# Kernel tuning notes

Measured on AMD Instinct MI355X. Metric: run time of the kernel, lower is better.

Reference implementation:

```python
import jax, jax.numpy as jnp
import numpy as np

H = 128   # hidden_size
DYN = 2   # dynamic_features


def setup_inputs() -> dict:
    B, S, STAT = 256, 64, 2
    key = jax.random.key(0)
    ks = jax.random.split(key, 9)
    sc = 0.05
    return {
        "static": jax.random.normal(ks[0], (B, STAT, S), jnp.float32),
        "static_embeddings": jax.random.normal(ks[1], (B, H, S), jnp.float32),
        "dynamic": jax.random.uniform(ks[2], (B, DYN, S), jnp.float32),
        # dynamic_embedding: Conv1d(2 -> 128, k=1)
        "dyn_w": jax.random.normal(ks[3], (H, DYN), jnp.float32) * sc,
        "dyn_b": jnp.zeros((H,), jnp.float32),
        # decoder_input_dynamic_embedding: Conv1d(128 -> 128, k=1)
        "in_w": jax.random.normal(ks[4], (H, H), jnp.float32) * sc,
        "in_b": jnp.zeros((H,), jnp.float32),
        # GRU (single layer, batch_first), torch gate order r,z,n
        "w_ih": jax.random.normal(ks[5], (3 * H, H), jnp.float32) * sc,
        "w_hh": jax.random.normal(ks[6], (3 * H, H), jnp.float32) * sc,
        "b_ih": jnp.zeros((3 * H,), jnp.float32),
        "b_hh": jnp.zeros((3 * H,), jnp.float32),
        # DoubleAttention: scores = v . tanh(W [static; dynamic; hidden])
        "W_att": jax.random.normal(ks[7], (H, 3 * H), jnp.float32) * sc,
        "v_att": jax.random.normal(ks[8], (H,), jnp.float32) * sc,
    }


def _pointer_forward(static_embeddings, dynamic, dyn_w, dyn_b, in_w, in_b,
                     w_ih, w_hh, b_ih, b_hh, W_att, v_att):
    B, Hd, S = static_embeddings.shape
    NEG = jnp.asarray(-1e9, static_embeddings.dtype)
    base = jax.random.key(42)

    def gru_cell(x, h):  # torch nn.GRU single step
        gi = x @ w_ih.T + b_ih
        gh = h @ w_hh.T + b_hh
        ir, iz, i_n = jnp.split(gi, 3, axis=-1)
        hr, hz, h_n = jnp.split(gh, 3, axis=-1)
        r = jax.nn.sigmoid(ir + hr)
        z = jax.nn.sigmoid(iz + hz)
        n = jnp.tanh(i_n + r * h_n)
        return (1.0 - z) * n + z * h

    first_mask = jnp.zeros((B, S), static_embeddings.dtype).at[:, 0].set(1.0)

    def step(carry, i):
        dec_in, h, visited, dyn = carry
        # decoder_input_dynamic_embedding: 1x1 conv == per-token linear
        x = dec_in @ in_w.T + in_b                      # [B,H]
        h = gru_cell(x, h)                              # decoder_output == new hidden
        # i==0: only depot (index 0) is selectable; afterwards: unvisited nodes
        mask = jnp.where(i == 0, first_mask, 1.0 - visited)
        dyn_emb = jnp.einsum('bds,hd->bhs', dyn, dyn_w) + dyn_b[None, :, None]
        ctx = jnp.concatenate(
            [static_embeddings, dyn_emb,
             jnp.broadcast_to(h[:, :, None], (B, Hd, S))], axis=1)  # [B,3H,S]
        scores = jnp.einsum('h,bhs->bs', v_att,
                            jnp.tanh(jnp.einsum('hk,bks->bhs', W_att, ctx)))
        logits = jnp.where(mask > 0, scores, NEG)       # -inf on masked positions
        ptr = jax.random.categorical(jax.random.fold_in(base, i), logits)  # sample
        logp = jnp.take_along_axis(jax.nn.log_softmax(logits, -1),
                                   ptr[:, None], axis=1)[:, 0]
        sel = (jnp.arange(S)[None, :] == ptr[:, None]).astype(dyn.dtype)  # [B,S]
        visited = jnp.maximum(visited, sel)
        dyn = dyn * (1.0 - sel)[:, None, :]             # update_dynamic_state
        # original feeds the (conv-transformed) decoder input back to itself
        return (x, h, visited, dyn), (ptr, logp)

    init = (static_embeddings[:, :, 0],                  # decoder_input = emb of node 0
            jnp.zeros((B, Hd), static_embeddings.dtype),  # GRU hidden
            jnp.zeros((B, S), static_embeddings.dtype),   # visited
            dynamic)
    _, (tours, logps) = jax.lax.scan(step, init, jnp.arange(S))
    return tours.T, logps.T  # [B,S], [B,S]


def reference(static, static_embeddings, dynamic, dyn_w, dyn_b, in_w, in_b,
              w_ih, w_hh, b_ih, b_hh, W_att, v_att):
    # dropout layers are identity in eval mode; `static` is only used for logging
    return _pointer_forward(static_embeddings, dynamic, dyn_w, dyn_b, in_w, in_b,
                            w_ih, w_hh, b_ih, b_hh, W_att, v_att)
```

## Files before the change

kernel.cpp:

```cpp
#include <hip/hip_runtime.h>
#include <stdint.h>


#define BN 256
#define SN 64
#define HN 128
#define NEGV (-1.0e9f)
#define TINYF 1.17549435e-38f

#define OFF_A   0
#define OFF_GI  8192
#define OFF_WHC 8192
#define OFF_SET 16384
#define OFF_UT  24832
#define OFF_HC  33280
#define OFF_KK  33536
#define OFF_SV  33664
#define OFF_DY  33792
#define OFF_WD  33920
#define OFF_CV  34176
#define SMEM_FLOATS 34304

__device__ __forceinline__ uint32_t rotl32(uint32_t v, int d) {
  return (v << d) | (v >> (32 - d));
}

__device__ __forceinline__ void threefry2x32(uint32_t k0, uint32_t k1,
                                             uint32_t x0, uint32_t x1,
                                             uint32_t& o0, uint32_t& o1) {
  uint32_t ks2 = k0 ^ k1 ^ 0x1BD11BDAu;
  x0 += k0; x1 += k1;
  x0 += x1; x1 = rotl32(x1, 13); x1 ^= x0;
  x0 += x1; x1 = rotl32(x1, 15); x1 ^= x0;
  x0 += x1; x1 = rotl32(x1, 26); x1 ^= x0;
  x0 += x1; x1 = rotl32(x1, 6);  x1 ^= x0;
  x0 += k1; x1 += ks2 + 1u;
  x0 += x1; x1 = rotl32(x1, 17); x1 ^= x0;
  x0 += x1; x1 = rotl32(x1, 29); x1 ^= x0;
  x0 += x1; x1 = rotl32(x1, 16); x1 ^= x0;
  x0 += x1; x1 = rotl32(x1, 24); x1 ^= x0;
  x0 += ks2; x1 += k0 + 2u;
  x0 += x1; x1 = rotl32(x1, 13); x1 ^= x0;
  x0 += x1; x1 = rotl32(x1, 15); x1 ^= x0;
  x0 += x1; x1 = rotl32(x1, 26); x1 ^= x0;
  x0 += x1; x1 = rotl32(x1, 6);  x1 ^= x0;
  x0 += k0; x1 += k1 + 3u;
  x0 += x1; x1 = rotl32(x1, 17); x1 ^= x0;
  x0 += x1; x1 = rotl32(x1, 29); x1 ^= x0;
  x0 += x1; x1 = rotl32(x1, 16); x1 ^= x0;
  x0 += x1; x1 = rotl32(x1, 24); x1 ^= x0;
  x0 += k1; x1 += ks2 + 4u;
  x0 += x1; x1 = rotl32(x1, 13); x1 ^= x0;
  x0 += x1; x1 = rotl32(x1, 15); x1 ^= x0;
  x0 += x1; x1 = rotl32(x1, 26); x1 ^= x0;
  x0 += x1; x1 = rotl32(x1, 6);  x1 ^= x0;
  x0 += ks2; x1 += k0 + 5u;
  o0 = x0; o1 = x1;
}

__device__ __forceinline__ float jax_gumbel(uint32_t k0, uint32_t k1, int j) {
  uint32_t o0, o1;
  threefry2x32(k0, k1, 0u, (uint32_t)j, o0, o1);
  uint32_t bits = o0 ^ o1;
  uint32_t ub = (bits >> 9) | 0x3F800000u;
  float u = __uint_as_float(ub) - 1.0f;
  u = fmaxf(u + TINYF, TINYF);
  return -logf(-logf(u));
}

__device__ __forceinline__ float ftanh(float x) {
  float ax = fabsf(x);
  float e = __expf(-2.0f * ax);
  float r = (1.0f - e) * __builtin_amdgcn_rcpf(1.0f + e);
  return copysignf(r, x);
}

__device__ __forceinline__ float fsig(float x) {
  return __builtin_amdgcn_rcpf(1.0f + __expf(-x));
}

__global__ void k0_dyn(const float* __restrict__ W_att, const float* __restrict__ dyn_w,
                       const float* __restrict__ dyn_b, float* __restrict__ Wd,
                       float* __restrict__ cv) {
  int h = threadIdx.x;
  float w0 = 0.f, w1 = 0.f, cc = 0.f;
  for (int k = 0; k < HN; ++k) {
    float w = W_att[h * 384 + 128 + k];
    w0 = fmaf(w, dyn_w[2 * k + 0], w0);
    w1 = fmaf(w, dyn_w[2 * k + 1], w1);
    cc = fmaf(w, dyn_b[k], cc);
  }
  Wd[2 * h] = w0; Wd[2 * h + 1] = w1; cv[h] = cc;
}

__global__ __launch_bounds__(512)
__attribute__((amdgpu_waves_per_eu(2, 2)))
void mega(
    const float* __restrict__ SE, const float* __restrict__ dynamic,
    const float* __restrict__ in_w, const float* __restrict__ in_b,
    const float* __restrict__ w_ih, const float* __restrict__ b_ih,
    const float* __restrict__ w_hh, const float* __restrict__ b_hh,
    const float* __restrict__ W_att, const float* __restrict__ v_att,
    const float* __restrict__ Wd, const float* __restrict__ cv,
    float* __restrict__ out) {
  extern __shared__ float sm[];
  int b = blockIdx.x, t = threadIdx.x;
  float* A   = sm + OFF_A;
  float* GIl = sm + OFF_GI;
  float* WHC = sm + OFF_WHC;
  float* SET = sm + OFF_SET;
  float* UT  = sm + OFF_UT;
  float* HC  = sm + OFF_HC;
  uint32_t* KK = (uint32_t*)(sm + OFF_KK);
  float* SV  = sm + OFF_SV;
  float* DY  = sm + OFF_DY;
  float* WDs = sm + OFF_WD;
  float* CVs = sm + OFF_CV;

  if (t < 64) {
    uint32_t o0, o1;
    threefry2x32(0u, 42u, 0u, (uint32_t)t, o0, o1);
    KK[2 * t] = o0; KK[2 * t + 1] = o1;
  }
  if (t < 128) {
    SV[t]  = v_att[t];
    DY[t]  = dynamic[b * 128 + t];
    CVs[t] = cv[t];
    HC[t]  = SE[b * 8192 + t * 64];
  }
  if (t < 256) WDs[t] = Wd[t];
  __syncthreads();

  {
    int ml = t >> 2, ks = t & 3;
    float4 wv[8];
#pragma unroll
    for (int q = 0; q < 8; ++q)
      wv[q] = *(const float4*)(in_w + ml * HN + q * 16 + ks * 4);
    float bib = in_b[ml];
    for (int ii = 0; ii < SN; ++ii) {
      const float* xc = HC + (ii & 1) * 128;
      float* xn = HC + ((ii + 1) & 1) * 128;
      float a0 = 0.f, a1 = 0.f, a2 = 0.f, a3 = 0.f;
#pragma unroll
      for (int q = 0; q < 8; ++q) {
        float4 x4 = *(const float4*)(xc + q * 16 + ks * 4);
        a0 = fmaf(wv[q].x, x4.x, a0);
        a1 = fmaf(wv[q].y, x4.y, a1);
        a2 = fmaf(wv[q].z, x4.z, a2);
        a3 = fmaf(wv[q].w, x4.w, a3);
      }
      float s = (a0 + a1) + (a2 + a3);
      s += __shfl_xor(s, 1); s += __shfl_xor(s, 2);
      if (ks == 0) {
        float xv = s + bib;
        A[ii * 128 + ml] = xv;
        xn[ml] = xv;
      }
      __syncthreads();
    }
  }

  {
    int ml = t >> 2, ks = t & 3;
    float4 wv[3][8]; float bi[3];
#pragma unroll
    for (int j = 0; j < 3; ++j) {
#pragma unroll
      for (int q = 0; q < 8; ++q)
        wv[j][q] = *(const float4*)(w_ih + (ml + 128 * j) * HN + q * 16 + ks * 4);
      bi[j] = b_ih[ml + 128 * j];
    }
    for (int n = 0; n < SN; ++n) {
      float4 x4[8];
#pragma unroll
      for (int q = 0; q < 8; ++q)
        x4[q] = *(const float4*)(A + n * 128 + q * 16 + ks * 4);
      float sum[3];
#pragma unroll
      for (int j = 0; j < 3; ++j) {
        float a0 = 0.f, a1 = 0.f, a2 = 0.f, a3 = 0.f;
#pragma unroll
        for (int q = 0; q < 8; ++q) {
          a0 = fmaf(wv[j][q].x, x4[q].x, a0);
          a1 = fmaf(wv[j][q].y, x4[q].y, a1);
          a2 = fmaf(wv[j][q].z, x4[q].z, a2);
          a3 = fmaf(wv[j][q].w, x4[q].w, a3);
        }
        float s = (a0 + a1) + (a2 + a3);
        s += __shfl_xor(s, 1); s += __shfl_xor(s, 2);
        sum[j] = s + bi[j];
      }
      if (ks == 0) {
#pragma unroll
        for (int j = 0; j < 3; ++j) GIl[n * 384 + ml + 128 * j] = sum[j];
      }
    }
    __syncthreads();
  }

  if (t < 256) HC[t] = 0.f;
  __syncthreads();
  {
    int ml = t >> 2, ks = t & 3;
    float4 wv[3][8]; float bh[3];
#pragma unroll
    for (int j = 0; j < 3; ++j) {
#pragma unroll
      for (int q = 0; q < 8; ++q)
        wv[j][q] = *(const float4*)(w_hh + (ml + 128 * j) * HN + q * 16 + ks * 4);
      bh[j] = b_hh[ml + 128 * j];
    }
    float hp = 0.f;
    for (int ii = 0; ii < SN; ++ii) {
      const float* hcr = HC + (ii & 1) * 128;
      float* hcw = HC + ((ii + 1) & 1) * 128;
      float4 x4[8];
#pragma unroll
      for (int q = 0; q < 8; ++q)
        x4[q] = *(const float4*)(hcr + q * 16 + ks * 4);
      float sum[3];
#pragma unroll
      for (int j = 0; j < 3; ++j) {
        float a0 = 0.f, a1 = 0.f, a2 = 0.f, a3 = 0.f;
#pragma unroll
        for (int q = 0; q < 8; ++q) {
          a0 = fmaf(wv[j][q].x, x4[q].x, a0);
          a1 = fmaf(wv[j][q].y, x4[q].y, a1);
          a2 = fmaf(wv[j][q].z, x4[q].z, a2);
          a3 = fmaf(wv[j][q].w, x4[q].w, a3);
        }
        float s = (a0 + a1) + (a2 + a3);
        s += __shfl_xor(s, 1); s += __shfl_xor(s, 2);
        sum[j] = s + bh[j];
      }
      if (ks == 0) {
        const float* gr = GIl + ii * 384;
        float r = fsig(gr[ml] + sum[0]);
        float z = fsig(gr[128 + ml] + sum[1]);
        float nn = ftanh(gr[256 + ml] + r * sum[2]);
        float hn = (1.0f - z) * nn + z * hp;
        hcw[ml] = hn;
        A[ii * 128 + ml] = hn;
        hp = hn;
      }
      __syncthreads();
    }
  }

  {
    int ml = t >> 3, ks = t & 7;
    float4 w0[4], w1[4];
#pragma unroll
    for (int q = 0; q < 4; ++q) {
      w0[q] = *(const float4*)(W_att + (ml)      * 384 + 256 + q * 32 + ks * 4);
      w1[q] = *(const float4*)(W_att + (ml + 64) * 384 + 256 + q * 32 + ks * 4);
    }
    for (int n = 0; n < SN; ++n) {
      float4 x4[4];
#pragma unroll
      for (int q = 0; q < 4; ++q)
        x4[q] = *(const float4*)(A + n * 128 + q * 32 + ks * 4);
      float a00 = 0.f, a01 = 0.f, a10 = 0.f, a11 = 0.f;
#pragma unroll
      for (int q = 0; q < 4; ++q) {
        a00 = fmaf(w0[q].x, x4[q].x, a00);
        a01 = fmaf(w0[q].y, x4[q].y, a01);
        a00 = fmaf(w0[q].z, x4[q].z, a00);
        a01 = fmaf(w0[q].w, x4[q].w, a01);
        a10 = fmaf(w1[q].x, x4[q].x, a10);
        a11 = fmaf(w1[q].y, x4[q].y, a11);
        a10 = fmaf(w1[q].z, x4[q].z, a10);
        a11 = fmaf(w1[q].w, x4[q].w, a11);
      }
      float s0 = a00 + a01, s1 = a10 + a11;
      s0 += __shfl_xor(s0, 1); s0 += __shfl_xor(s0, 2); s0 += __shfl_xor(s0, 4);
      s1 += __shfl_xor(s1, 1); s1 += __shfl_xor(s1, 2); s1 += __shfl_xor(s1, 4);
      if (ks == 0) { WHC[n * 128 + ml] = s0; WHC[n * 128 + ml + 64] = s1; }
    }
    __syncthreads();
  }

  for (int p = 0; p < 16; ++p) {
    int idx = p * 512 + t;
    int h = idx >> 6, s = idx & 63;
    SET[s * 132 + h] = SE[b * 8192 + idx];
  }
  __syncthreads();

  {
    int ml = t >> 3, ks = t & 7;
    float4 w0[4], w1[4];
#pragma unroll
    for (int q = 0; q < 4; ++q) {
      w0[q] = *(const float4*)(W_att + (ml)      * 384 + q * 32 + ks * 4);
      w1[q] = *(const float4*)(W_att + (ml + 64) * 384 + q * 32 + ks * 4);
    }
    for (int n = 0; n < SN; ++n) {
      float4 x4[4];
#pragma unroll
      for (int q = 0; q < 4; ++q)
        x4[q] = *(const float4*)(SET + n * 132 + q * 32 + ks * 4);
      float a00 = 0.f, a01 = 0.f, a10 = 0.f, a11 = 0.f;
#pragma unroll
      for (int q = 0; q < 4; ++q) {
        a00 = fmaf(w0[q].x, x4[q].x, a00);
        a01 = fmaf(w0[q].y, x4[q].y, a01);
        a00 = fmaf(w0[q].z, x4[q].z, a00);
        a01 = fmaf(w0[q].w, x4[q].w, a01);
        a10 = fmaf(w1[q].x, x4[q].x, a10);
        a11 = fmaf(w1[q].y, x4[q].y, a11);
        a10 = fmaf(w1[q].z, x4[q].z, a10);
        a11 = fmaf(w1[q].w, x4[q].w, a11);
      }
      float s0 = a00 + a01, s1 = a10 + a11;
      s0 += __shfl_xor(s0, 1); s0 += __shfl_xor(s0, 2); s0 += __shfl_xor(s0, 4);
      s1 += __shfl_xor(s1, 1); s1 += __shfl_xor(s1, 2); s1 += __shfl_xor(s1, 4);
      if (ks == 0) {
        float d0 = DY[n], d1 = DY[64 + n];
        UT[(ml)      * 66 + n] = s0 + WDs[2 * ml] * d0 + WDs[2 * ml + 1] * d1 + CVs[ml];
        UT[(ml + 64) * 66 + n] = s1 + WDs[2 * (ml + 64)] * d0 + WDs[2 * (ml + 64) + 1] * d1 + CVs[ml + 64];
      }
    }
    __syncthreads();
  }

  {
    int s = t & 63, w = t >> 6;
    float acc[8];
#pragma unroll
    for (int j = 0; j < 8; ++j) acc[j] = 0.f;
    for (int h = 0; h < HN; h += 4) {
      float u0 = UT[(h + 0) * 66 + s];
      float u1 = UT[(h + 1) * 66 + s];
      float u2 = UT[(h + 2) * 66 + s];
      float u3 = UT[(h + 3) * 66 + s];
      float4 v4 = *(const float4*)(SV + h);
#pragma unroll
      for (int j = 0; j < 8; ++j) {
        float4 wh = *(const float4*)(WHC + (w * 8 + j) * 128 + h);
        float a = acc[j];
        a = fmaf(v4.x, ftanh(u0 + wh.x), a);
        a = fmaf(v4.y, ftanh(u1 + wh.y), a);
        a = fmaf(v4.z, ftanh(u2 + wh.z), a);
        a = fmaf(v4.w, ftanh(u3 + wh.w), a);
        acc[j] = a;
      }
    }
    __syncthreads();
#pragma unroll
    for (int j = 0; j < 8; ++j) A[(w * 8 + j) * 64 + s] = acc[j];
    __syncthreads();
  }

  {
    float* G = A + 4096;
    for (int p = 0; p < 8; ++p) {
      int idx = p * 512 + t;
      int i = idx >> 6;
      G[idx] = jax_gumbel(KK[2 * i], KK[2 * i + 1], b * 64 + (idx & 63));
    }
    __syncthreads();
  }

  if (t < 64) {
    const float* Pl = A;
    const float* Gl = A + 4096;
    int s = t;
    bool visited = false;
    for (int i = 0; i < SN; ++i) {
      float score = Pl[i * 64 + s];
      bool allowed = (i == 0) ? (s == 0) : (!visited);
      float logit = allowed ? score : NEGV;
      float z = logit + Gl[i * 64 + s];
      float bz = z; int bi = s;
#pragma unroll
      for (int off = 32; off > 0; off >>= 1) {
        float oz = __shfl_xor(bz, off);
        int oi = __shfl_xor(bi, off);
        if (oz > bz || (oz == bz && oi < bi)) { bz = oz; bi = oi; }
      }
      int ptr = bi;
      float m = logit;
#pragma unroll
      for (int off = 32; off > 0; off >>= 1) m = fmaxf(m, __shfl_xor(m, off));
      float e = expf(logit - m);
      float sum = e;
#pragma unroll
      for (int off = 32; off > 0; off >>= 1) sum += __shfl_xor(sum, off);
      float chosen = __shfl(logit, ptr);
      float logp = (chosen - m) - logf(sum);
      if (s == ptr) visited = true;
      if (s == 0) {
        out[b * SN + i] = (float)ptr;
        out[BN * SN + b * SN + i] = logp;
      }
    }
  }
}

extern "C" void kernel_launch(void* const* d_in, const int* in_sizes, int n_in,
                              void* d_out, int out_size, void* d_ws, size_t ws_size,
                              hipStream_t stream) {
  const float* SE    = (const float*)d_in[1];
  const float* dynam = (const float*)d_in[2];
  const float* dyn_w = (const float*)d_in[3];
  const float* dyn_b = (const float*)d_in[4];
  const float* in_w  = (const float*)d_in[5];
  const float* in_b  = (const float*)d_in[6];
  const float* w_ih  = (const float*)d_in[7];
  const float* b_ih  = (const float*)d_in[8 - 1];
  const float* w_hh  = (const float*)d_in[8];
  const float* b_ih2 = (const float*)d_in[9];
  const float* b_hh  = (const float*)d_in[10];
  const float* W_att = (const float*)d_in[11];
  const float* v_att = (const float*)d_in[12];
  float* out = (float*)d_out;
  float* ws = (float*)d_ws;

  float* Wd = ws;
  float* cv = ws + 256;

  (void)hipFuncSetAttribute((const void*)mega,
                            hipFuncAttributeMaxDynamicSharedMemorySize,
                            SMEM_FLOATS * 4);

  hipLaunchKernelGGL(k0_dyn, dim3(1), dim3(128), 0, stream,
                     W_att, dyn_w, dyn_b, Wd, cv);
  hipLaunchKernelGGL(mega, dim3(BN), dim3(512), SMEM_FLOATS * 4, stream,
                     SE, dynam, in_w, in_b, w_ih, b_ih2, w_hh, b_hh,
                     W_att, v_att, Wd, cv, out);
}
```

Measured before the change: 317.9 us.

## Double block size to 1024 threads and split each dot product across 8 lanes

Launches the per-batch mega kernel with 1024 threads instead of 512 and re-partitions every matvec phase. Each output row now gets 8 lanes, each holding 4 float4 weight registers, with a three-stage shuffle reduction. The attention projections compute one row per thread group instead of two, and the score loop handles 4 query rows per wave instead of 8. The aim is to halve per-thread work and register load in the serial GRU and input-conv recurrences, which are latency bound. The cost is barriers across 16 waves instead of 8 and an extra shuffle stage per reduction.

```diff
diff --git a/kernel.cpp b/kernel.cpp
--- a/kernel.cpp
+++ b/kernel.cpp
@@ -93,9 +93,7 @@
   Wd[2 * h] = w0; Wd[2 * h + 1] = w1; cv[h] = cc;
 }
 
-__global__ __launch_bounds__(512)
-__attribute__((amdgpu_waves_per_eu(2, 2)))
-void mega(
+__global__ __launch_bounds__(1024) void mega(
     const float* __restrict__ SE, const float* __restrict__ dynamic,
     const float* __restrict__ in_w, const float* __restrict__ in_b,
     const float* __restrict__ w_ih, const float* __restrict__ b_ih,
@@ -117,6 +115,8 @@
   float* WDs = sm + OFF_WD;
   float* CVs = sm + OFF_CV;
 
+  int ml = t >> 3, ks = t & 7;
+
   if (t < 64) {
     uint32_t o0, o1;
     threefry2x32(0u, 42u, 0u, (uint32_t)t, o0, o1);
@@ -132,26 +132,25 @@
   __syncthreads();
 
   {
-    int ml = t >> 2, ks = t & 3;
-    float4 wv[8];
-#pragma unroll
-    for (int q = 0; q < 8; ++q)
-      wv[q] = *(const float4*)(in_w + ml * HN + q * 16 + ks * 4);
+    float4 wv[4];
+#pragma unroll
+    for (int q = 0; q < 4; ++q)
+      wv[q] = *(const float4*)(in_w + ml * HN + q * 32 + ks * 4);
     float bib = in_b[ml];
     for (int ii = 0; ii < SN; ++ii) {
       const float* xc = HC + (ii & 1) * 128;
       float* xn = HC + ((ii + 1) & 1) * 128;
       float a0 = 0.f, a1 = 0.f, a2 = 0.f, a3 = 0.f;
 #pragma unroll
-      for (int q = 0; q < 8; ++q) {
-        float4 x4 = *(const float4*)(xc + q * 16 + ks * 4);
+      for (int q = 0; q < 4; ++q) {
+        float4 x4 = *(const float4*)(xc + q * 32 + ks * 4);
         a0 = fmaf(wv[q].x, x4.x, a0);
         a1 = fmaf(wv[q].y, x4.y, a1);
         a2 = fmaf(wv[q].z, x4.z, a2);
         a3 = fmaf(wv[q].w, x4.w, a3);
       }
       float s = (a0 + a1) + (a2 + a3);
-      s += __shfl_xor(s, 1); s += __shfl_xor(s, 2);
+      s += __shfl_xor(s, 1); s += __shfl_xor(s, 2); s += __shfl_xor(s, 4);
       if (ks == 0) {
         float xv = s + bib;
         A[ii * 128 + ml] = xv;
@@ -162,33 +161,32 @@
   }
 
   {
-    int ml = t >> 2, ks = t & 3;
-    float4 wv[3][8]; float bi[3];
+    float4 wv[3][4]; float bi[3];
 #pragma unroll
     for (int j = 0; j < 3; ++j) {
 #pragma unroll
-      for (int q = 0; q < 8; ++q)
-        wv[j][q] = *(const float4*)(w_ih + (ml + 128 * j) * HN + q * 16 + ks * 4);
+      for (int q = 0; q < 4; ++q)
+        wv[j][q] = *(const float4*)(w_ih + (ml + 128 * j) * HN + q * 32 + ks * 4);
       bi[j] = b_ih[ml + 128 * j];
     }
     for (int n = 0; n < SN; ++n) {
-      float4 x4[8];
-#pragma unroll
-      for (int q = 0; q < 8; ++q)
-        x4[q] = *(const float4*)(A + n * 128 + q * 16 + ks * 4);
+      float4 x4[4];
+#pragma unroll
+      for (int q = 0; q < 4; ++q)
+        x4[q] = *(const float4*)(A + n * 128 + q * 32 + ks * 4);
       float sum[3];
 #pragma unroll
       for (int j = 0; j < 3; ++j) {
         float a0 = 0.f, a1 = 0.f, a2 = 0.f, a3 = 0.f;
 #pragma unroll
-        for (int q = 0; q < 8; ++q) {
+        for (int q = 0; q < 4; ++q) {
           a0 = fmaf(wv[j][q].x, x4[q].x, a0);
           a1 = fmaf(wv[j][q].y, x4[q].y, a1);
           a2 = fmaf(wv[j][q].z, x4[q].z, a2);
           a3 = fmaf(wv[j][q].w, x4[q].w, a3);
         }
         float s = (a0 + a1) + (a2 + a3);
-        s += __shfl_xor(s, 1); s += __shfl_xor(s, 2);
+        s += __shfl_xor(s, 1); s += __shfl_xor(s, 2); s += __shfl_xor(s, 4);
         sum[j] = s + bi[j];
       }
       if (ks == 0) {
@@ -202,36 +200,35 @@
   if (t < 256) HC[t] = 0.f;
   __syncthreads();
   {
-    int ml = t >> 2, ks = t & 3;
-    float4 wv[3][8]; float bh[3];
+    float4 wv[3][4]; float bh[3];
 #pragma unroll
     for (int j = 0; j < 3; ++j) {
 #pragma unroll
-      for (int q = 0; q < 8; ++q)
-        wv[j][q] = *(const float4*)(w_hh + (ml + 128 * j) * HN + q * 16 + ks * 4);
+      for (int q = 0; q < 4; ++q)
+        wv[j][q] = *(const float4*)(w_hh + (ml + 128 * j) * HN + q * 32 + ks * 4);
       bh[j] = b_hh[ml + 128 * j];
     }
     float hp = 0.f;
     for (int ii = 0; ii < SN; ++ii) {
       const float* hcr = HC + (ii & 1) * 128;
       float* hcw = HC + ((ii + 1) & 1) * 128;
-      float4 x4[8];
-#pragma unroll
-      for (int q = 0; q < 8; ++q)
-        x4[q] = *(const float4*)(hcr + q * 16 + ks * 4);
+      float4 x4[4];
+#pragma unroll
+      for (int q = 0; q < 4; ++q)
+        x4[q] = *(const float4*)(hcr + q * 32 + ks * 4);
       float sum[3];
 #pragma unroll
       for (int j = 0; j < 3; ++j) {
         float a0 = 0.f, a1 = 0.f, a2 = 0.f, a3 = 0.f;
 #pragma unroll
-        for (int q = 0; q < 8; ++q) {
+        for (int q = 0; q < 4; ++q) {
           a0 = fmaf(wv[j][q].x, x4[q].x, a0);
           a1 = fmaf(wv[j][q].y, x4[q].y, a1);
           a2 = fmaf(wv[j][q].z, x4[q].z, a2);
           a3 = fmaf(wv[j][q].w, x4[q].w, a3);
         }
         float s = (a0 + a1) + (a2 + a3);
-        s += __shfl_xor(s, 1); s += __shfl_xor(s, 2);
+        s += __shfl_xor(s, 1); s += __shfl_xor(s, 2); s += __shfl_xor(s, 4);
         sum[j] = s + bh[j];
       }
       if (ks == 0) {
@@ -249,77 +246,56 @@
   }
 
   {
-    int ml = t >> 3, ks = t & 7;
-    float4 w0[4], w1[4];
-#pragma unroll
-    for (int q = 0; q < 4; ++q) {
-      w0[q] = *(const float4*)(W_att + (ml)      * 384 + 256 + q * 32 + ks * 4);
-      w1[q] = *(const float4*)(W_att + (ml + 64) * 384 + 256 + q * 32 + ks * 4);
-    }
+    float4 wv[4];
+#pragma unroll
+    for (int q = 0; q < 4; ++q)
+      wv[q] = *(const float4*)(W_att + ml * 384 + 256 + q * 32 + ks * 4);
     for (int n = 0; n < SN; ++n) {
-      float4 x4[4];
-#pragma unroll
-      for (int q = 0; q < 4; ++q)
-        x4[q] = *(const float4*)(A + n * 128 + q * 32 + ks * 4);
-      float a00 = 0.f, a01 = 0.f, a10 = 0.f, a11 = 0.f;
+      float a0 = 0.f, a1 = 0.f, a2 = 0.f, a3 = 0.f;
 #pragma unroll
       for (int q = 0; q < 4; ++q) {
-        a00 = fmaf(w0[q].x, x4[q].x, a00);
-        a01 = fmaf(w0[q].y, x4[q].y, a01);
-        a00 = fmaf(w0[q].z, x4[q].z, a00);
-        a01 = fmaf(w0[q].w, x4[q].w, a01);
-        a10 = fmaf(w1[q].x, x4[q].x, a10);
-        a11 = fmaf(w1[q].y, x4[q].y, a11);
-        a10 = fmaf(w1[q].z, x4[q].z, a10);
-        a11 = fmaf(w1[q].w, x4[q].w, a11);
-      }
-      float s0 = a00 + a01, s1 = a10 + a11;
-      s0 += __shfl_xor(s0, 1); s0 += __shfl_xor(s0, 2); s0 += __shfl_xor(s0, 4);
-      s1 += __shfl_xor(s1, 1); s1 += __shfl_xor(s1, 2); s1 += __shfl_xor(s1, 4);
-      if (ks == 0) { WHC[n * 128 + ml] = s0; WHC[n * 128 + ml + 64] = s1; }
-    }
-    __syncthreads();
-  }
-
-  for (int p = 0; p < 16; ++p) {
-    int idx = p * 512 + t;
+        float4 x4 = *(const float4*)(A + n * 128 + q * 32 + ks * 4);
+        a0 = fmaf(wv[q].x, x4.x, a0);
+        a1 = fmaf(wv[q].y, x4.y, a1);
+        a2 = fmaf(wv[q].z, x4.z, a2);
+        a3 = fmaf(wv[q].w, x4.w, a3);
+      }
+      float s = (a0 + a1) + (a2 + a3);
+      s += __shfl_xor(s, 1); s += __shfl_xor(s, 2); s += __shfl_xor(s, 4);
+      if (ks == 0) WHC[n * 128 + ml] = s;
+    }
+    __syncthreads();
+  }
+
+#pragma unroll
+  for (int p = 0; p < 8; ++p) {
+    int idx = p * 1024 + t;
     int h = idx >> 6, s = idx & 63;
     SET[s * 132 + h] = SE[b * 8192 + idx];
   }
   __syncthreads();
 
   {
-    int ml = t >> 3, ks = t & 7;
-    float4 w0[4], w1[4];
-#pragma unroll
-    for (int q = 0; q < 4; ++q) {
-      w0[q] = *(const float4*)(W_att + (ml)      * 384 + q * 32 + ks * 4);
-      w1[q] = *(const float4*)(W_att + (ml + 64) * 384 + q * 32 + ks * 4);
-    }
+    float4 wv[4];
+#pragma unroll
+    for (int q = 0; q < 4; ++q)
+      wv[q] = *(const float4*)(W_att + ml * 384 + q * 32 + ks * 4);
+    float wd0 = WDs[2 * ml], wd1 = WDs[2 * ml + 1], cvm = CVs[ml];
     for (int n = 0; n < SN; ++n) {
-      float4 x4[4];
-#pragma unroll
-      for (int q = 0; q < 4; ++q)
-        x4[q] = *(const float4*)(SET + n * 132 + q * 32 + ks * 4);
-      float a00 = 0.f, a01 = 0.f, a10 = 0.f, a11 = 0.f;
+      float a0 = 0.f, a1 = 0.f, a2 = 0.f, a3 = 0.f;
 #pragma unroll
       for (int q = 0; q < 4; ++q) {
-        a00 = fmaf(w0[q].x, x4[q].x, a00);
-        a01 = fmaf(w0[q].y, x4[q].y, a01);
-        a00 = fmaf(w0[q].z, x4[q].z, a00);
-        a01 = fmaf(w0[q].w, x4[q].w, a01);
-        a10 = fmaf(w1[q].x, x4[q].x, a10);
-        a11 = fmaf(w1[q].y, x4[q].y, a11);
-        a10 = fmaf(w1[q].z, x4[q].z, a10);
-        a11 = fmaf(w1[q].w, x4[q].w, a11);
-      }
-      float s0 = a00 + a01, s1 = a10 + a11;
-      s0 += __shfl_xor(s0, 1); s0 += __shfl_xor(s0, 2); s0 += __shfl_xor(s0, 4);
-      s1 += __shfl_xor(s1, 1); s1 += __shfl_xor(s1, 2); s1 += __shfl_xor(s1, 4);
+        float4 x4 = *(const float4*)(SET + n * 132 + q * 32 + ks * 4);
+        a0 = fmaf(wv[q].x, x4.x, a0);
+        a1 = fmaf(wv[q].y, x4.y, a1);
+        a2 = fmaf(wv[q].z, x4.z, a2);
+        a3 = fmaf(wv[q].w, x4.w, a3);
+      }
+      float s = (a0 + a1) + (a2 + a3);
+      s += __shfl_xor(s, 1); s += __shfl_xor(s, 2); s += __shfl_xor(s, 4);
       if (ks == 0) {
         float d0 = DY[n], d1 = DY[64 + n];
-        UT[(ml)      * 66 + n] = s0 + WDs[2 * ml] * d0 + WDs[2 * ml + 1] * d1 + CVs[ml];
-        UT[(ml + 64) * 66 + n] = s1 + WDs[2 * (ml + 64)] * d0 + WDs[2 * (ml + 64) + 1] * d1 + CVs[ml + 64];
+        UT[ml * 66 + n] = s + wd0 * d0 + wd1 * d1 + cvm;
       }
     }
     __syncthreads();
@@ -327,9 +303,9 @@
 
   {
     int s = t & 63, w = t >> 6;
-    float acc[8];
-#pragma unroll
-    for (int j = 0; j < 8; ++j) acc[j] = 0.f;
+    float acc[4];
+#pragma unroll
+    for (int j = 0; j < 4; ++j) acc[j] = 0.f;
     for (int h = 0; h < HN; h += 4) {
       float u0 = UT[(h + 0) * 66 + s];
       float u1 = UT[(h + 1) * 66 + s];
@@ -337,8 +313,8 @@
       float u3 = UT[(h + 3) * 66 + s];
       float4 v4 = *(const float4*)(SV + h);
 #pragma unroll
-      for (int j = 0; j < 8; ++j) {
-        float4 wh = *(const float4*)(WHC + (w * 8 + j) * 128 + h);
+      for (int j = 0; j < 4; ++j) {
+        float4 wh = *(const float4*)(WHC + (w * 4 + j) * 128 + h);
         float a = acc[j];
         a = fmaf(v4.x, ftanh(u0 + wh.x), a);
         a = fmaf(v4.y, ftanh(u1 + wh.y), a);
@@ -349,14 +325,15 @@
     }
     __syncthreads();
 #pragma unroll
-    for (int j = 0; j < 8; ++j) A[(w * 8 + j) * 64 + s] = acc[j];
+    for (int j = 0; j < 4; ++j) A[(w * 4 + j) * 64 + s] = acc[j];
     __syncthreads();
   }
 
   {
     float* G = A + 4096;
-    for (int p = 0; p < 8; ++p) {
-      int idx = p * 512 + t;
+#pragma unroll
+    for (int p = 0; p < 4; ++p) {
+      int idx = p * 1024 + t;
       int i = idx >> 6;
       G[idx] = jax_gumbel(KK[2 * i], KK[2 * i + 1], b * 64 + (idx & 63));
     }
@@ -409,9 +386,8 @@
   const float* in_w  = (const float*)d_in[5];
   const float* in_b  = (const float*)d_in[6];
   const float* w_ih  = (const float*)d_in[7];
-  const float* b_ih  = (const float*)d_in[8 - 1];
   const float* w_hh  = (const float*)d_in[8];
-  const float* b_ih2 = (const float*)d_in[9];
+  const float* b_ih  = (const float*)d_in[9];
   const float* b_hh  = (const float*)d_in[10];
   const float* W_att = (const float*)d_in[11];
   const float* v_att = (const float*)d_in[12];
@@ -427,7 +403,7 @@
 
   hipLaunchKernelGGL(k0_dyn, dim3(1), dim3(128), 0, stream,
                      W_att, dyn_w, dyn_b, Wd, cv);
-  hipLaunchKernelGGL(mega, dim3(BN), dim3(512), SMEM_FLOATS * 4, stream,
-                     SE, dynam, in_w, in_b, w_ih, b_ih2, w_hh, b_hh,
+  hipLaunchKernelGGL(mega, dim3(BN), dim3(1024), SMEM_FLOATS * 4, stream,
+                     SE, dynam, in_w, in_b, w_ih, b_ih, w_hh, b_hh,
                      W_att, v_att, Wd, cv, out);
 }
```

New measurement: 347.3 us. 1.09x slower.

## Split fused megakernel into staged kernels with global intermediates and 2-way attention grid

Applied to the files above, without the earlier changes.

Breaks the single per-batch megakernel into four kernels (input/GRU recurrence, attention projections, tanh-score plus gumbel, sampling) that pass intermediates through global workspace. The score stage runs on a grid with two blocks per batch, and the GRU input projection is reorganised into four K-chunks so fewer weight registers stay live. Key generation moves into the setup kernel. The goal is lower per-kernel shared memory and register pressure and more parallel blocks for the heavy tanh stage, at the cost of extra launches and global round-trips.

```diff
diff --git a/kernel.cpp b/kernel.cpp
--- a/kernel.cpp
+++ b/kernel.cpp
@@ -7,19 +7,6 @@
 #define HN 128
 #define NEGV (-1.0e9f)
 #define TINYF 1.17549435e-38f
-
-#define OFF_A   0
-#define OFF_GI  8192
-#define OFF_WHC 8192
-#define OFF_SET 16384
-#define OFF_UT  24832
-#define OFF_HC  33280
-#define OFF_KK  33536
-#define OFF_SV  33664
-#define OFF_DY  33792
-#define OFF_WD  33920
-#define OFF_CV  34176
-#define SMEM_FLOATS 34304
 
 __device__ __forceinline__ uint32_t rotl32(uint32_t v, int d) {
   return (v << d) | (v >> (32 - d));
@@ -81,8 +68,13 @@
 
 __global__ void k0_dyn(const float* __restrict__ W_att, const float* __restrict__ dyn_w,
                        const float* __restrict__ dyn_b, float* __restrict__ Wd,
-                       float* __restrict__ cv) {
+                       float* __restrict__ cv, uint32_t* __restrict__ keys) {
   int h = threadIdx.x;
+  if (h < 64) {
+    uint32_t o0, o1;
+    threefry2x32(0u, 42u, 0u, (uint32_t)h, o0, o1);
+    keys[2 * h] = o0; keys[2 * h + 1] = o1;
+  }
   float w0 = 0.f, w1 = 0.f, cc = 0.f;
   for (int k = 0; k < HN; ++k) {
     float w = W_att[h * 384 + 128 + k];
@@ -95,40 +87,17 @@
 
 __global__ __launch_bounds__(512)
 __attribute__((amdgpu_waves_per_eu(2, 2)))
-void mega(
-    const float* __restrict__ SE, const float* __restrict__ dynamic,
-    const float* __restrict__ in_w, const float* __restrict__ in_b,
-    const float* __restrict__ w_ih, const float* __restrict__ b_ih,
-    const float* __restrict__ w_hh, const float* __restrict__ b_hh,
-    const float* __restrict__ W_att, const float* __restrict__ v_att,
-    const float* __restrict__ Wd, const float* __restrict__ cv,
-    float* __restrict__ out) {
+void kA(const float* __restrict__ SE,
+        const float* __restrict__ in_w, const float* __restrict__ in_b,
+        const float* __restrict__ w_ih, const float* __restrict__ b_ih,
+        const float* __restrict__ w_hh, const float* __restrict__ b_hh,
+        float* __restrict__ H_g) {
   extern __shared__ float sm[];
+  float* A   = sm;
+  float* GIl = sm + 8192;
+  float* HC  = sm + 32768;
   int b = blockIdx.x, t = threadIdx.x;
-  float* A   = sm + OFF_A;
-  float* GIl = sm + OFF_GI;
-  float* WHC = sm + OFF_WHC;
-  float* SET = sm + OFF_SET;
-  float* UT  = sm + OFF_UT;
-  float* HC  = sm + OFF_HC;
-  uint32_t* KK = (uint32_t*)(sm + OFF_KK);
-  float* SV  = sm + OFF_SV;
-  float* DY  = sm + OFF_DY;
-  float* WDs = sm + OFF_WD;
-  float* CVs = sm + OFF_CV;
-
-  if (t < 64) {
-    uint32_t o0, o1;
-    threefry2x32(0u, 42u, 0u, (uint32_t)t, o0, o1);
-    KK[2 * t] = o0; KK[2 * t + 1] = o1;
-  }
-  if (t < 128) {
-    SV[t]  = v_att[t];
-    DY[t]  = dynamic[b * 128 + t];
-    CVs[t] = cv[t];
-    HC[t]  = SE[b * 8192 + t * 64];
-  }
-  if (t < 256) WDs[t] = Wd[t];
+  if (t < 128) HC[t] = SE[b * 8192 + t * 64];
   __syncthreads();
 
   {
@@ -163,37 +132,39 @@
 
   {
     int ml = t >> 2, ks = t & 3;
-    float4 wv[3][8]; float bi[3];
-#pragma unroll
-    for (int j = 0; j < 3; ++j) {
-#pragma unroll
-      for (int q = 0; q < 8; ++q)
-        wv[j][q] = *(const float4*)(w_ih + (ml + 128 * j) * HN + q * 16 + ks * 4);
-      bi[j] = b_ih[ml + 128 * j];
-    }
-    for (int n = 0; n < SN; ++n) {
-      float4 x4[8];
-#pragma unroll
-      for (int q = 0; q < 8; ++q)
-        x4[q] = *(const float4*)(A + n * 128 + q * 16 + ks * 4);
-      float sum[3];
-#pragma unroll
-      for (int j = 0; j < 3; ++j) {
-        float a0 = 0.f, a1 = 0.f, a2 = 0.f, a3 = 0.f;
-#pragma unroll
-        for (int q = 0; q < 8; ++q) {
-          a0 = fmaf(wv[j][q].x, x4[q].x, a0);
-          a1 = fmaf(wv[j][q].y, x4[q].y, a1);
-          a2 = fmaf(wv[j][q].z, x4[q].z, a2);
-          a3 = fmaf(wv[j][q].w, x4[q].w, a3);
+    float bi[3];
+#pragma unroll
+    for (int j = 0; j < 3; ++j) bi[j] = b_ih[ml + 128 * j];
+#pragma unroll
+    for (int p = 0; p < 4; ++p) {
+      float4 wv[3][2];
+#pragma unroll
+      for (int j = 0; j < 3; ++j)
+#pragma unroll
+        for (int q = 0; q < 2; ++q)
+          wv[j][q] = *(const float4*)(w_ih + (ml + 128 * j) * HN + p * 32 + q * 16 + ks * 4);
+      for (int n = 0; n < SN; ++n) {
+        float4 x0 = *(const float4*)(A + n * 128 + p * 32 + ks * 4);
+        float4 x1 = *(const float4*)(A + n * 128 + p * 32 + 16 + ks * 4);
+#pragma unroll
+        for (int j = 0; j < 3; ++j) {
+          float a0 = fmaf(wv[j][0].x, x0.x, 0.f);
+          float a1 = fmaf(wv[j][0].y, x0.y, 0.f);
+          float a2 = fmaf(wv[j][0].z, x0.z, 0.f);
+          float a3 = fmaf(wv[j][0].w, x0.w, 0.f);
+          a0 = fmaf(wv[j][1].x, x1.x, a0);
+          a1 = fmaf(wv[j][1].y, x1.y, a1);
+          a2 = fmaf(wv[j][1].z, x1.z, a2);
+          a3 = fmaf(wv[j][1].w, x1.w, a3);
+          float s = (a0 + a1) + (a2 + a3);
+          s += __shfl_xor(s, 1); s += __shfl_xor(s, 2);
+          if (ks == 0) {
+            int idx = n * 384 + ml + 128 * j;
+            if (p == 0) GIl[idx] = s;
+            else if (p == 3) GIl[idx] = GIl[idx] + s + bi[j];
+            else GIl[idx] += s;
+          }
         }
-        float s = (a0 + a1) + (a2 + a3);
-        s += __shfl_xor(s, 1); s += __shfl_xor(s, 2);
-        sum[j] = s + bi[j];
-      }
-      if (ks == 0) {
-#pragma unroll
-        for (int j = 0; j < 3; ++j) GIl[n * 384 + ml + 128 * j] = sum[j];
       }
     }
     __syncthreads();
@@ -241,12 +212,29 @@
         float nn = ftanh(gr[256 + ml] + r * sum[2]);
         float hn = (1.0f - z) * nn + z * hp;
         hcw[ml] = hn;
-        A[ii * 128 + ml] = hn;
+        H_g[(b * SN + ii) * HN + ml] = hn;
         hp = hn;
       }
       __syncthreads();
     }
   }
+}
+
+__global__ __launch_bounds__(512) void kB(
+    const float* __restrict__ SE, const float* __restrict__ dynamic,
+    const float* __restrict__ W_att,
+    const float* __restrict__ Wd, const float* __restrict__ cv,
+    const float* __restrict__ H_g,
+    float* __restrict__ WHC_g, float* __restrict__ UT_g) {
+  extern __shared__ float sm[];
+  float* A   = sm;
+  float* SET = sm + 8192;
+  float* UT  = sm + 16640;
+  int b = blockIdx.x, t = threadIdx.x;
+#pragma unroll
+  for (int p = 0; p < 4; ++p)
+    ((float4*)A)[p * 512 + t] = ((const float4*)(H_g + b * 8192))[p * 512 + t];
+  __syncthreads();
 
   {
     int ml = t >> 3, ks = t & 7;
@@ -276,9 +264,11 @@
       float s0 = a00 + a01, s1 = a10 + a11;
       s0 += __shfl_xor(s0, 1); s0 += __shfl_xor(s0, 2); s0 += __shfl_xor(s0, 4);
       s1 += __shfl_xor(s1, 1); s1 += __shfl_xor(s1, 2); s1 += __shfl_xor(s1, 4);
-      if (ks == 0) { WHC[n * 128 + ml] = s0; WHC[n * 128 + ml + 64] = s1; }
-    }
-    __syncthreads();
+      if (ks == 0) {
+        WHC_g[(b * SN + n) * HN + ml] = s0;
+        WHC_g[(b * SN + n) * HN + ml + 64] = s1;
+      }
+    }
   }
 
   for (int p = 0; p < 16; ++p) {
@@ -317,55 +307,74 @@
       s0 += __shfl_xor(s0, 1); s0 += __shfl_xor(s0, 2); s0 += __shfl_xor(s0, 4);
       s1 += __shfl_xor(s1, 1); s1 += __shfl_xor(s1, 2); s1 += __shfl_xor(s1, 4);
       if (ks == 0) {
-        float d0 = DY[n], d1 = DY[64 + n];
-        UT[(ml)      * 66 + n] = s0 + WDs[2 * ml] * d0 + WDs[2 * ml + 1] * d1 + CVs[ml];
-        UT[(ml + 64) * 66 + n] = s1 + WDs[2 * (ml + 64)] * d0 + WDs[2 * (ml + 64) + 1] * d1 + CVs[ml + 64];
+        float d0 = dynamic[b * 128 + n], d1 = dynamic[b * 128 + 64 + n];
+        UT[(ml)      * 66 + n] = s0 + Wd[2 * ml] * d0 + Wd[2 * ml + 1] * d1 + cv[ml];
+        UT[(ml + 64) * 66 + n] = s1 + Wd[2 * (ml + 64)] * d0 + Wd[2 * (ml + 64) + 1] * d1 + cv[ml + 64];
       }
     }
     __syncthreads();
   }
-
-  {
-    int s = t & 63, w = t >> 6;
-    float acc[8];
-#pragma unroll
-    for (int j = 0; j < 8; ++j) acc[j] = 0.f;
-    for (int h = 0; h < HN; h += 4) {
-      float u0 = UT[(h + 0) * 66 + s];
-      float u1 = UT[(h + 1) * 66 + s];
-      float u2 = UT[(h + 2) * 66 + s];
-      float u3 = UT[(h + 3) * 66 + s];
-      float4 v4 = *(const float4*)(SV + h);
-#pragma unroll
-      for (int j = 0; j < 8; ++j) {
-        float4 wh = *(const float4*)(WHC + (w * 8 + j) * 128 + h);
-        float a = acc[j];
-        a = fmaf(v4.x, ftanh(u0 + wh.x), a);
-        a = fmaf(v4.y, ftanh(u1 + wh.y), a);
-        a = fmaf(v4.z, ftanh(u2 + wh.z), a);
-        a = fmaf(v4.w, ftanh(u3 + wh.w), a);
-        acc[j] = a;
-      }
-    }
-    __syncthreads();
-#pragma unroll
-    for (int j = 0; j < 8; ++j) A[(w * 8 + j) * 64 + s] = acc[j];
-    __syncthreads();
-  }
-
-  {
-    float* G = A + 4096;
-    for (int p = 0; p < 8; ++p) {
-      int idx = p * 512 + t;
-      int i = idx >> 6;
-      G[idx] = jax_gumbel(KK[2 * i], KK[2 * i + 1], b * 64 + (idx & 63));
-    }
-    __syncthreads();
-  }
-
+  for (int idx = t; idx < 8448; idx += 512) UT_g[b * 8448 + idx] = UT[idx];
+}
+
+__global__ __launch_bounds__(256) void kC(
+    const float* __restrict__ UT_g, const float* __restrict__ WHC_g,
+    const float* __restrict__ v_att, const uint32_t* __restrict__ keys,
+    float* __restrict__ P_g, float* __restrict__ G_g) {
+  __shared__ float UTl[8448];
+  __shared__ float WH[32 * HN];
+  __shared__ float SVl[HN];
+  int b = blockIdx.x, y = blockIdx.y, t = threadIdx.x;
+  for (int idx = t; idx < 8448; idx += 256) UTl[idx] = UT_g[b * 8448 + idx];
+  for (int idx = t; idx < 4096; idx += 256)
+    WH[idx] = WHC_g[(b * SN + y * 32) * HN + idx];
+  if (t < HN) SVl[t] = v_att[t];
+  __syncthreads();
+  int s = t & 63, w = t >> 6;
+  float acc[8];
+#pragma unroll
+  for (int j = 0; j < 8; ++j) acc[j] = 0.f;
+  for (int h = 0; h < HN; h += 4) {
+    float u0 = UTl[(h + 0) * 66 + s];
+    float u1 = UTl[(h + 1) * 66 + s];
+    float u2 = UTl[(h + 2) * 66 + s];
+    float u3 = UTl[(h + 3) * 66 + s];
+    float4 v4 = *(const float4*)(SVl + h);
+#pragma unroll
+    for (int j = 0; j < 8; ++j) {
+      float4 wh = *(const float4*)(WH + (w * 8 + j) * HN + h);
+      float a = acc[j];
+      a = fmaf(v4.x, ftanh(u0 + wh.x), a);
+      a = fmaf(v4.y, ftanh(u1 + wh.y), a);
+      a = fmaf(v4.z, ftanh(u2 + wh.z), a);
+      a = fmaf(v4.w, ftanh(u3 + wh.w), a);
+      acc[j] = a;
+    }
+  }
+#pragma unroll
+  for (int j = 0; j < 8; ++j)
+    P_g[b * 4096 + (y * 32 + w * 8 + j) * 64 + s] = acc[j];
+  for (int p = 0; p < 8; ++p) {
+    int idx = p * 256 + t;
+    int i = y * 32 + (idx >> 6);
+    int s2 = idx & 63;
+    G_g[b * 4096 + i * 64 + s2] = jax_gumbel(keys[2 * i], keys[2 * i + 1], b * 64 + s2);
+  }
+}
+
+__global__ __launch_bounds__(256) void kD(const float* __restrict__ P_g,
+                                          const float* __restrict__ G_g,
+                                          float* __restrict__ out) {
+  __shared__ float Pl[4096];
+  __shared__ float Gl[4096];
+  int b = blockIdx.x, t = threadIdx.x;
+#pragma unroll
+  for (int p = 0; p < 4; ++p) {
+    ((float4*)Pl)[p * 256 + t] = ((const float4*)(P_g + b * 4096))[p * 256 + t];
+    ((float4*)Gl)[p * 256 + t] = ((const float4*)(G_g + b * 4096))[p * 256 + t];
+  }
+  __syncthreads();
   if (t < 64) {
-    const float* Pl = A;
-    const float* Gl = A + 4096;
     int s = t;
     bool visited = false;
     for (int i = 0; i < SN; ++i) {
@@ -409,25 +418,35 @@
   const float* in_w  = (const float*)d_in[5];
   const float* in_b  = (const float*)d_in[6];
   const float* w_ih  = (const float*)d_in[7];
-  const float* b_ih  = (const float*)d_in[8 - 1];
   const float* w_hh  = (const float*)d_in[8];
-  const float* b_ih2 = (const float*)d_in[9];
+  const float* b_ih  = (const float*)d_in[9];
   const float* b_hh  = (const float*)d_in[10];
   const float* W_att = (const float*)d_in[11];
   const float* v_att = (const float*)d_in[12];
   float* out = (float*)d_out;
   float* ws = (float*)d_ws;
 
-  float* Wd = ws;
-  float* cv = ws + 256;
-
-  (void)hipFuncSetAttribute((const void*)mega,
-                            hipFuncAttributeMaxDynamicSharedMemorySize,
-                            SMEM_FLOATS * 4);
+  float* H_g   = ws;
+  float* P_g   = ws;
+  float* G_g   = ws + 1048576;
+  float* WHC_g = ws + 2097152;
+  float* UT_g  = ws + 4194304;
+  float* Wd    = ws + 6356992;
+  float* cv    = Wd + 256;
+  uint32_t* keys = (uint32_t*)(cv + 128);
+
+  (void)hipFuncSetAttribute((const void*)kA,
+                            hipFuncAttributeMaxDynamicSharedMemorySize, 132096);
+  (void)hipFuncSetAttribute((const void*)kB,
+                            hipFuncAttributeMaxDynamicSharedMemorySize, 100352);
 
   hipLaunchKernelGGL(k0_dyn, dim3(1), dim3(128), 0, stream,
-                     W_att, dyn_w, dyn_b, Wd, cv);
-  hipLaunchKernelGGL(mega, dim3(BN), dim3(512), SMEM_FLOATS * 4, stream,
-                     SE, dynam, in_w, in_b, w_ih, b_ih2, w_hh, b_hh,
-                     W_att, v_att, Wd, cv, out);
-}
+                     W_att, dyn_w, dyn_b, Wd, cv, keys);
+  hipLaunchKernelGGL(kA, dim3(BN), dim3(512), 132096, stream,
+                     SE, in_w, in_b, w_ih, b_ih, w_hh, b_hh, H_g);
+  hipLaunchKernelGGL(kB, dim3(BN), dim3(512), 100352, stream,
+                     SE, dynam, W_att, Wd, cv, H_g, WHC_g, UT_g);
+  hipLaunchKernelGGL(kC, dim3(BN, 2), dim3(256), 0, stream,
+                     UT_g, WHC_g, v_att, keys, P_g, G_g);
+  hipLaunchKernelGGL(kD, dim3(BN), dim3(256), 0, stream, P_g, G_g, out);
+}
```

After: 408.9 us. +28.6%, slower.
